# Kernel optimization log

Measured on AMD Instinct MI355X. Metric: run time of the kernel, lower is better.

Reference implementation:

```python
import jax, jax.numpy as jnp
from jax import lax
import numpy as np

SIGMA = 5.0
ALPHA = 50.0
RADIUS = int(4.0 * SIGMA + 0.5)  # scipy gaussian_filter truncate=4.0 -> 20


def _gauss_kernel():
    t = jnp.arange(-RADIUS, RADIUS + 1, dtype=jnp.float32)
    phi = jnp.exp(-0.5 * (t / SIGMA) ** 2)
    return phi / phi.sum()


def _gaussian_blur(f):
    # f: [B, H, W]. scipy mode='reflect' (edge included) == jnp.pad mode='symmetric'.
    k = _gauss_kernel()
    K = 2 * RADIUS + 1
    fp = jnp.pad(f, ((0, 0), (RADIUS, RADIUS), (RADIUS, RADIUS)), mode='symmetric')[:, None]
    z = lax.conv_general_dilated(fp, k.reshape(1, 1, K, 1), (1, 1), 'VALID')
    z = lax.conv_general_dilated(z, k.reshape(1, 1, 1, K), (1, 1), 'VALID')
    return z[:, 0]


def _reflect(i, n):
    # scipy mode='reflect': (d c b a | a b c d | d c b a), period 2n on integer indices
    i = jnp.mod(i, 2 * n)
    return jnp.where(i >= n, 2 * n - 1 - i, i)


def _bilinear(img, yy, xx):
    # img: [H, W]; yy/xx: [H, W] float sample coords (rows, cols)
    H, W = img.shape
    y0 = jnp.floor(yy)
    x0 = jnp.floor(xx)
    wy = yy - y0
    wx = xx - x0
    y0i = y0.astype(jnp.int32)
    x0i = x0.astype(jnp.int32)
    y0r = _reflect(y0i, H)
    y1r = _reflect(y0i + 1, H)
    x0r = _reflect(x0i, W)
    x1r = _reflect(x0i + 1, W)
    v00 = img[y0r, x0r]
    v01 = img[y0r, x1r]
    v10 = img[y1r, x0r]
    v11 = img[y1r, x1r]
    return (v00 * (1 - wy) * (1 - wx) + v01 * (1 - wy) * wx
            + v10 * wy * (1 - wx) + v11 * wy * wx)


def setup_inputs() -> dict:
    key = jax.random.key(0)
    k1, k2, k3 = jax.random.split(key, 3)
    B, H, W = 64, 512, 512
    x = jax.random.normal(k1, (B, 1, H, W), dtype=jnp.float32)
    rand_dx = jax.random.uniform(k2, (B, H, W), dtype=jnp.float32)
    rand_dy = jax.random.uniform(k3, (B, H, W), dtype=jnp.float32)
    return {"x": x, "rand_dx": rand_dx, "rand_dy": rand_dy}


def reference(x, rand_dx, rand_dy):
    # x: [B, 1, H, W]
    B, C, H, W = x.shape
    dx = _gaussian_blur(rand_dx * 2.0 - 1.0) * ALPHA  # [B, H, W]
    dy = _gaussian_blur(rand_dy * 2.0 - 1.0) * ALPHA
    gx, gy = jnp.meshgrid(jnp.arange(W, dtype=x.dtype), jnp.arange(H, dtype=x.dtype))
    yy = gy[None] + dy  # row coords
    xx = gx[None] + dx  # col coords
    warped = jax.vmap(_bilinear)(x[:, 0], yy, xx)  # [B, H, W]
    return warped[:, None]
```

## Files before the change

kernel.cpp:

```cpp
#include <hip/hip_runtime.h>

#define RADIUS 20
#define KSIZE  41
#define ALPHA_F 50.0f
#define TY     16
#define WID    512
#define HEI    512
#define PW     (WID + 2 * RADIUS)
#define NRH    48
#define PF     8

__device__ constexpr float G[KSIZE] = {
    2.6770e-05f, 5.8390e-05f, 1.22380e-04f, 2.46460e-04f, 4.76840e-04f,
    8.86410e-04f, 1.583160e-03f, 2.716710e-03f, 4.479090e-03f, 7.095210e-03f,
    1.0798630e-02f, 1.5790680e-02f, 2.2185070e-02f, 2.9946720e-02f, 3.8838800e-02f,
    4.8396120e-02f, 5.7940680e-02f, 6.6647650e-02f, 7.3657040e-02f, 7.8211730e-02f,
    7.9791720e-02f,
    7.8211730e-02f, 7.3657040e-02f, 6.6647650e-02f, 5.7940680e-02f, 4.8396120e-02f,
    3.8838800e-02f, 2.9946720e-02f, 2.2185070e-02f, 1.5790680e-02f, 1.0798630e-02f,
    7.095210e-03f, 4.479090e-03f, 2.716710e-03f, 1.583160e-03f, 8.86410e-04f,
    4.76840e-04f, 2.46460e-04f, 1.22380e-04f, 5.8390e-05f, 2.6770e-05f
};

__device__ __forceinline__ int refl(int i, int n) {
    i = (i < 0) ? (-1 - i) : i;
    i = (i >= n) ? (2 * n - 1 - i) : i;
    return i;
}

__device__ __forceinline__ int refl512(int i) {
    i = (i < 0) ? (-1 - i) : i;
    return (i >= 512) ? (1023 - i) : i;
}

template<bool INTERIOR>
__device__ __forceinline__ void vblur8(const float* __restrict__ src, int ybase,
                                       float acc[8][4]) {
    float bx[PF][4];
    #pragma unroll
    for (int k = 0; k < PF; ++k) {
        const int gy = INTERIOR ? (ybase + k) : refl(ybase + k, HEI);
        const float4 v = *reinterpret_cast<const float4*>(src + (size_t)gy * WID);
        bx[k][0] = v.x; bx[k][1] = v.y; bx[k][2] = v.z; bx[k][3] = v.w;
    }
    #pragma unroll
    for (int r = 0; r < NRH; ++r) {
        float v[4];
        #pragma unroll
        for (int j = 0; j < 4; ++j) v[j] = bx[r & (PF - 1)][j];
        if (r + PF < NRH) {
            const int gy = INTERIOR ? (ybase + r + PF) : refl(ybase + r + PF, HEI);
            const float4 nv = *reinterpret_cast<const float4*>(src + (size_t)gy * WID);
            bx[r & (PF - 1)][0] = nv.x; bx[r & (PF - 1)][1] = nv.y;
            bx[r & (PF - 1)][2] = nv.z; bx[r & (PF - 1)][3] = nv.w;
        }
        #pragma unroll
        for (int o = 0; o < 8; ++o) {
            const int t = r - o;
            if (t >= 0 && t < KSIZE) {
                const float g = G[t];
                #pragma unroll
                for (int j = 0; j < 4; ++j) acc[o][j] = fmaf(g, v[j], acc[o][j]);
            }
        }
    }
}

__global__ __launch_bounds__(512) void elastic_kernel(
    const float* __restrict__ xin, const float* __restrict__ rdx,
    const float* __restrict__ rdy, float* __restrict__ outp, int B) {

    __shared__ float sdx[TY][PW];
    __shared__ float sdy[TY][PW];

    const int tid = threadIdx.x;

    int b, band;
    {
        const int L = blockIdx.x;
        if (B == 64) {
            const int xcd = L & 7;
            const int s   = L >> 3;
            b    = xcd * 8 + (s >> 5);
            band = s & 31;
        } else {
            b    = L / (HEI / TY);
            band = L % (HEI / TY);
        }
    }
    const int y0 = band * TY;
    const size_t base = (size_t)b * (HEI * WID);

    {
        const int c4 = tid & 127;
        const int f  = (tid >> 7) & 1;
        const int h  = tid >> 8;
        const int ybase = y0 + 8 * h - RADIUS;

        const float* src = (f ? rdy : rdx) + base + 4 * c4;

        float acc[8][4];
        #pragma unroll
        for (int o = 0; o < 8; ++o)
            #pragma unroll
            for (int j = 0; j < 4; ++j) acc[o][j] = 0.f;

        if (ybase >= 0 && ybase + NRH <= HEI) vblur8<true >(src, ybase, acc);
        else                                  vblur8<false>(src, ybase, acc);

        float (*sd)[PW] = f ? sdy : sdx;

        #pragma unroll
        for (int o = 0; o < 8; ++o) {
            const int row = 8 * h + o;
            float sv[4];
            #pragma unroll
            for (int j = 0; j < 4; ++j) sv[j] = 2.f * acc[o][j] - 1.f;
            float4 pack;
            pack.x = sv[0]; pack.y = sv[1]; pack.z = sv[2]; pack.w = sv[3];
            *reinterpret_cast<float4*>(&sd[row][RADIUS + 4 * c4]) = pack;
            if (c4 < 5) {
                #pragma unroll
                for (int j = 0; j < 4; ++j) sd[row][RADIUS - 1 - (4 * c4 + j)] = sv[j];
            }
            if (c4 >= 123) {
                #pragma unroll
                for (int j = 0; j < 4; ++j) sd[row][RADIUS + 2 * WID - 1 - (4 * c4 + j)] = sv[j];
            }
        }
    }
    __syncthreads();

    const int c4 = tid & 127;
    const int rg = tid >> 7;
    const float* img = xin + base;

    #pragma unroll
    for (int i = 0; i < 4; ++i) {
        const int o  = rg + 4 * i;
        const int gy = y0 + o;

        float dxv[4] = {0.f, 0.f, 0.f, 0.f};
        float dyv[4] = {0.f, 0.f, 0.f, 0.f};

        {
            float w[44];
            const float4* rp = (const float4*)(&sdx[o][0]);
            #pragma unroll
            for (int q = 0; q < 11; ++q) {
                const float4 v = rp[c4 + q];
                w[4 * q + 0] = v.x; w[4 * q + 1] = v.y;
                w[4 * q + 2] = v.z; w[4 * q + 3] = v.w;
            }
            #pragma unroll
            for (int t = 0; t < KSIZE; ++t) {
                const float g = G[t];
                #pragma unroll
                for (int j = 0; j < 4; ++j) dxv[j] = fmaf(g, w[t + j], dxv[j]);
            }
        }
        {
            float w[44];
            const float4* rp = (const float4*)(&sdy[o][0]);
            #pragma unroll
            for (int q = 0; q < 11; ++q) {
                const float4 v = rp[c4 + q];
                w[4 * q + 0] = v.x; w[4 * q + 1] = v.y;
                w[4 * q + 2] = v.z; w[4 * q + 3] = v.w;
            }
            #pragma unroll
            for (int t = 0; t < KSIZE; ++t) {
                const float g = G[t];
                #pragma unroll
                for (int j = 0; j < 4; ++j) dyv[j] = fmaf(g, w[t + j], dyv[j]);
            }
        }

        float st[4];
        #pragma unroll
        for (int j = 0; j < 4; ++j) {
            const int col = 4 * c4 + j;
            float xx = (float)col + dxv[j] * ALPHA_F;
            float yy = (float)gy  + dyv[j] * ALPHA_F;
            xx = fminf(fmaxf(xx, -511.f), 1022.f);
            yy = fminf(fmaxf(yy, -511.f), 1022.f);
            const float x0f = floorf(xx), y0f = floorf(yy);
            const float wx = xx - x0f, wy = yy - y0f;
            const int x0 = (int)x0f, yb = (int)y0f;
            const int x0r = refl512(x0);
            const int x1r = refl512(x0 + 1);
            const int y0r = refl512(yb);
            const int y1r = refl512(yb + 1);

            const float* r0 = img + ((size_t)y0r << 9);
            const float* r1 = img + ((size_t)y1r << 9);
            const float v00 = r0[x0r];
            const float v01 = r0[x1r];
            const float v10 = r1[x0r];
            const float v11 = r1[x1r];

            const float top = fmaf(wx, v01 - v00, v00);
            const float bot = fmaf(wx, v11 - v10, v10);
            st[j] = fmaf(wy, bot - top, top);
        }

        float4 pack;
        pack.x = st[0]; pack.y = st[1]; pack.z = st[2]; pack.w = st[3];
        *reinterpret_cast<float4*>(outp + base + (size_t)gy * WID + 4 * c4) = pack;
    }
}

extern "C" void kernel_launch(void* const* d_in, const int* in_sizes, int n_in,
                              void* d_out, int out_size, void* d_ws, size_t ws_size,
                              hipStream_t stream) {
    const float* x   = (const float*)d_in[0];
    const float* rdx = (const float*)d_in[1];
    const float* rdy = (const float*)d_in[2];
    float* out = (float*)d_out;

    const int B = in_sizes[1] / (HEI * WID);

    const int nblocks = B * (HEI / TY);
    elastic_kernel<<<nblocks, 512, 0, stream>>>(x, rdx, rdy, out, B);
    (void)d_ws; (void)ws_size; (void)n_in; (void)out_size;
}
```

Baseline: 286.2 us.

## Split band into two half-bands to halve shared memory and register pressure

The 16-row band is processed as two 8-row halves, each with its own vertical blur pass (4 output rows per thread), a sync, and the warp pass. This halves the LDS footprint and the vertical-blur accumulators, which may raise occupancy. In exchange, the vertical blur re-reads the overlapping halo rows for the second half. The horizontal blur also interleaves the x and y LDS reads directly into FMAs, and output stores become nontemporal.

```diff
diff --git a/kernel.cpp b/kernel.cpp
--- a/kernel.cpp
+++ b/kernel.cpp
@@ -4,11 +4,14 @@
 #define KSIZE  41
 #define ALPHA_F 50.0f
 #define TY     16
+#define HB     8
 #define WID    512
 #define HEI    512
 #define PW     (WID + 2 * RADIUS)
-#define NRH    48
+#define NRQ    44
 #define PF     8
+
+typedef float floatx4 __attribute__((ext_vector_type(4)));
 
 __device__ constexpr float G[KSIZE] = {
     2.6770e-05f, 5.8390e-05f, 1.22380e-04f, 2.46460e-04f, 4.76840e-04f,
@@ -34,28 +37,28 @@
 }
 
 template<bool INTERIOR>
-__device__ __forceinline__ void vblur8(const float* __restrict__ src, int ybase,
-                                       float acc[8][4]) {
-    float bx[PF][4];
+__device__ __forceinline__ void vblur4(const float* __restrict__ src, int ybase,
+                                       float acc[4][4]) {
+    float ring[PF][4];
     #pragma unroll
     for (int k = 0; k < PF; ++k) {
         const int gy = INTERIOR ? (ybase + k) : refl(ybase + k, HEI);
         const float4 v = *reinterpret_cast<const float4*>(src + (size_t)gy * WID);
-        bx[k][0] = v.x; bx[k][1] = v.y; bx[k][2] = v.z; bx[k][3] = v.w;
+        ring[k][0] = v.x; ring[k][1] = v.y; ring[k][2] = v.z; ring[k][3] = v.w;
     }
     #pragma unroll
-    for (int r = 0; r < NRH; ++r) {
+    for (int r = 0; r < NRQ; ++r) {
         float v[4];
         #pragma unroll
-        for (int j = 0; j < 4; ++j) v[j] = bx[r & (PF - 1)][j];
-        if (r + PF < NRH) {
+        for (int j = 0; j < 4; ++j) v[j] = ring[r & (PF - 1)][j];
+        if (r + PF < NRQ) {
             const int gy = INTERIOR ? (ybase + r + PF) : refl(ybase + r + PF, HEI);
             const float4 nv = *reinterpret_cast<const float4*>(src + (size_t)gy * WID);
-            bx[r & (PF - 1)][0] = nv.x; bx[r & (PF - 1)][1] = nv.y;
-            bx[r & (PF - 1)][2] = nv.z; bx[r & (PF - 1)][3] = nv.w;
+            ring[r & (PF - 1)][0] = nv.x; ring[r & (PF - 1)][1] = nv.y;
+            ring[r & (PF - 1)][2] = nv.z; ring[r & (PF - 1)][3] = nv.w;
         }
         #pragma unroll
-        for (int o = 0; o < 8; ++o) {
+        for (int o = 0; o < 4; ++o) {
             const int t = r - o;
             if (t >= 0 && t < KSIZE) {
                 const float g = G[t];
@@ -70,8 +73,8 @@
     const float* __restrict__ xin, const float* __restrict__ rdx,
     const float* __restrict__ rdy, float* __restrict__ outp, int B) {
 
-    __shared__ float sdx[TY][PW];
-    __shared__ float sdy[TY][PW];
+    __shared__ float sdx[HB][PW];
+    __shared__ float sdy[HB][PW];
 
     const int tid = threadIdx.x;
 
@@ -91,122 +94,117 @@
     const int y0 = band * TY;
     const size_t base = (size_t)b * (HEI * WID);
 
-    {
-        const int c4 = tid & 127;
-        const int f  = (tid >> 7) & 1;
-        const int h  = tid >> 8;
-        const int ybase = y0 + 8 * h - RADIUS;
-
-        const float* src = (f ? rdy : rdx) + base + 4 * c4;
-
-        float acc[8][4];
-        #pragma unroll
-        for (int o = 0; o < 8; ++o)
-            #pragma unroll
-            for (int j = 0; j < 4; ++j) acc[o][j] = 0.f;
-
-        if (ybase >= 0 && ybase + NRH <= HEI) vblur8<true >(src, ybase, acc);
-        else                                  vblur8<false>(src, ybase, acc);
-
-        float (*sd)[PW] = f ? sdy : sdx;
-
-        #pragma unroll
-        for (int o = 0; o < 8; ++o) {
-            const int row = 8 * h + o;
-            float sv[4];
-            #pragma unroll
-            for (int j = 0; j < 4; ++j) sv[j] = 2.f * acc[o][j] - 1.f;
-            float4 pack;
-            pack.x = sv[0]; pack.y = sv[1]; pack.z = sv[2]; pack.w = sv[3];
-            *reinterpret_cast<float4*>(&sd[row][RADIUS + 4 * c4]) = pack;
-            if (c4 < 5) {
-                #pragma unroll
-                for (int j = 0; j < 4; ++j) sd[row][RADIUS - 1 - (4 * c4 + j)] = sv[j];
-            }
-            if (c4 >= 123) {
-                #pragma unroll
-                for (int j = 0; j < 4; ++j) sd[row][RADIUS + 2 * WID - 1 - (4 * c4 + j)] = sv[j];
-            }
-        }
-    }
-    __syncthreads();
-
     const int c4 = tid & 127;
+    const int f  = (tid >> 7) & 1;
+    const int rq = tid >> 8;
+    const float* src = (f ? rdy : rdx) + base + 4 * c4;
+    float (*sd)[PW] = f ? sdy : sdx;
+
     const int rg = tid >> 7;
     const float* img = xin + base;
 
     #pragma unroll
-    for (int i = 0; i < 4; ++i) {
-        const int o  = rg + 4 * i;
-        const int gy = y0 + o;
-
-        float dxv[4] = {0.f, 0.f, 0.f, 0.f};
-        float dyv[4] = {0.f, 0.f, 0.f, 0.f};
+    for (int hb = 0; hb < 2; ++hb) {
+        const int yh = y0 + HB * hb;
 
         {
-            float w[44];
-            const float4* rp = (const float4*)(&sdx[o][0]);
+            const int ybase = yh + 4 * rq - RADIUS;
+
+            float acc[4][4];
+            #pragma unroll
+            for (int o = 0; o < 4; ++o)
+                #pragma unroll
+                for (int j = 0; j < 4; ++j) acc[o][j] = 0.f;
+
+            if (ybase >= 0 && ybase + NRQ <= HEI) vblur4<true >(src, ybase, acc);
+            else                                  vblur4<false>(src, ybase, acc);
+
+            #pragma unroll
+            for (int o = 0; o < 4; ++o) {
+                const int row = 4 * rq + o;
+                float sv[4];
+                #pragma unroll
+                for (int j = 0; j < 4; ++j) sv[j] = 2.f * acc[o][j] - 1.f;
+                float4 pack;
+                pack.x = sv[0]; pack.y = sv[1]; pack.z = sv[2]; pack.w = sv[3];
+                *reinterpret_cast<float4*>(&sd[row][RADIUS + 4 * c4]) = pack;
+                if (c4 < 5) {
+                    #pragma unroll
+                    for (int j = 0; j < 4; ++j) sd[row][RADIUS - 1 - (4 * c4 + j)] = sv[j];
+                }
+                if (c4 >= 123) {
+                    #pragma unroll
+                    for (int j = 0; j < 4; ++j) sd[row][RADIUS + 2 * WID - 1 - (4 * c4 + j)] = sv[j];
+                }
+            }
+        }
+        __syncthreads();
+
+        #pragma unroll
+        for (int i = 0; i < 2; ++i) {
+            const int o  = rg + 4 * i;
+            const int gy = yh + o;
+
+            float dxv[4] = {0.f, 0.f, 0.f, 0.f};
+            float dyv[4] = {0.f, 0.f, 0.f, 0.f};
+
+            const float4* rpx = (const float4*)(&sdx[o][0]);
+            const float4* rpy = (const float4*)(&sdy[o][0]);
             #pragma unroll
             for (int q = 0; q < 11; ++q) {
-                const float4 v = rp[c4 + q];
-                w[4 * q + 0] = v.x; w[4 * q + 1] = v.y;
-                w[4 * q + 2] = v.z; w[4 * q + 3] = v.w;
-            }
-            #pragma unroll
-            for (int t = 0; t < KSIZE; ++t) {
-                const float g = G[t];
-                #pragma unroll
-                for (int j = 0; j < 4; ++j) dxv[j] = fmaf(g, w[t + j], dxv[j]);
-            }
-        }
-        {
-            float w[44];
-            const float4* rp = (const float4*)(&sdy[o][0]);
-            #pragma unroll
-            for (int q = 0; q < 11; ++q) {
-                const float4 v = rp[c4 + q];
-                w[4 * q + 0] = v.x; w[4 * q + 1] = v.y;
-                w[4 * q + 2] = v.z; w[4 * q + 3] = v.w;
-            }
-            #pragma unroll
-            for (int t = 0; t < KSIZE; ++t) {
-                const float g = G[t];
-                #pragma unroll
-                for (int j = 0; j < 4; ++j) dyv[j] = fmaf(g, w[t + j], dyv[j]);
-            }
-        }
-
-        float st[4];
-        #pragma unroll
-        for (int j = 0; j < 4; ++j) {
-            const int col = 4 * c4 + j;
-            float xx = (float)col + dxv[j] * ALPHA_F;
-            float yy = (float)gy  + dyv[j] * ALPHA_F;
-            xx = fminf(fmaxf(xx, -511.f), 1022.f);
-            yy = fminf(fmaxf(yy, -511.f), 1022.f);
-            const float x0f = floorf(xx), y0f = floorf(yy);
-            const float wx = xx - x0f, wy = yy - y0f;
-            const int x0 = (int)x0f, yb = (int)y0f;
-            const int x0r = refl512(x0);
-            const int x1r = refl512(x0 + 1);
-            const int y0r = refl512(yb);
-            const int y1r = refl512(yb + 1);
-
-            const float* r0 = img + ((size_t)y0r << 9);
-            const float* r1 = img + ((size_t)y1r << 9);
-            const float v00 = r0[x0r];
-            const float v01 = r0[x1r];
-            const float v10 = r1[x0r];
-            const float v11 = r1[x1r];
-
-            const float top = fmaf(wx, v01 - v00, v00);
-            const float bot = fmaf(wx, v11 - v10, v10);
-            st[j] = fmaf(wy, bot - top, top);
-        }
-
-        float4 pack;
-        pack.x = st[0]; pack.y = st[1]; pack.z = st[2]; pack.w = st[3];
-        *reinterpret_cast<float4*>(outp + base + (size_t)gy * WID + 4 * c4) = pack;
+                const float4 vx = rpx[c4 + q];
+                const float4 vy = rpy[c4 + q];
+                const float ex[4] = {vx.x, vx.y, vx.z, vx.w};
+                const float ey[4] = {vy.x, vy.y, vy.z, vy.w};
+                #pragma unroll
+                for (int e = 0; e < 4; ++e) {
+                    const int k = 4 * q + e;
+                    #pragma unroll
+                    for (int j = 0; j < 4; ++j) {
+                        const int t = k - j;
+                        if (t >= 0 && t < KSIZE) {
+                            const float g = G[t];
+                            dxv[j] = fmaf(g, ex[e], dxv[j]);
+                            dyv[j] = fmaf(g, ey[e], dyv[j]);
+                        }
+                    }
+                }
+            }
+
+            float st[4];
+            #pragma unroll
+            for (int j = 0; j < 4; ++j) {
+                const int col = 4 * c4 + j;
+                float xx = (float)col + dxv[j] * ALPHA_F;
+                float yy = (float)gy  + dyv[j] * ALPHA_F;
+                xx = fminf(fmaxf(xx, -511.f), 1022.f);
+                yy = fminf(fmaxf(yy, -511.f), 1022.f);
+                const float x0f = floorf(xx), y0f = floorf(yy);
+                const float wx = xx - x0f, wy = yy - y0f;
+                const int x0 = (int)x0f, yb = (int)y0f;
+                const int x0r = refl512(x0);
+                const int x1r = refl512(x0 + 1);
+                const int y0r = refl512(yb);
+                const int y1r = refl512(yb + 1);
+
+                const float* r0 = img + ((size_t)y0r << 9);
+                const float* r1 = img + ((size_t)y1r << 9);
+                const float v00 = r0[x0r];
+                const float v01 = r0[x1r];
+                const float v10 = r1[x0r];
+                const float v11 = r1[x1r];
+
+                const float top = fmaf(wx, v01 - v00, v00);
+                const float bot = fmaf(wx, v11 - v10, v10);
+                st[j] = fmaf(wy, bot - top, top);
+            }
+
+            floatx4 pack;
+            pack.x = st[0]; pack.y = st[1]; pack.z = st[2]; pack.w = st[3];
+            __builtin_nontemporal_store(pack,
+                reinterpret_cast<floatx4*>(outp + base + (size_t)gy * WID + 4 * c4));
+        }
+        __syncthreads();
     }
 }
 
```

After: 312.9 us. +9.3%, slower.
